# Performance work log

Hardware: AMD Instinct MI355X
Metric: run time of the kernel (lower is better)

## Reference

```python
import jax, jax.numpy as jnp
import numpy as np

H = 16  # num_heads

def _rotate_half(x):
    x1, x2 = jnp.split(x, 2, axis=-1)
    return jnp.concatenate((-x2, x1), axis=-1)

def setup_inputs() -> dict:
    key = jax.random.key(0)
    ks = jax.random.split(key, 8)
    B, N, C = 4, 2048, 1024
    d = C // H
    x = jax.random.normal(ks[0], (B, N, C), dtype=jnp.float32)
    cos = jax.random.uniform(ks[1], (1, 1, N, d), dtype=jnp.float32)
    sin = jax.random.uniform(ks[2], (1, 1, N, d), dtype=jnp.float32)
    s = 0.02
    Wq = jax.random.normal(ks[3], (C, C), dtype=jnp.float32) * s
    Wkv = jax.random.normal(ks[4], (C, 2 * C), dtype=jnp.float32) * s
    Wout = jax.random.normal(ks[5], (C, C), dtype=jnp.float32) * s
    bout = jnp.zeros((C,), dtype=jnp.float32)
    return {"x": x, "cos": cos, "sin": sin, "Wq": Wq, "Wkv": Wkv, "Wout": Wout, "bout": bout}

def reference(x, cos, sin, Wq, Wkv, Wout, bout):
    B, N, C = x.shape
    d = C // H
    scale = d ** (-0.5)
    # projections (qkv_bias=False)
    q = (x @ Wq).reshape(B, N, H, d).transpose(0, 2, 1, 3)        # (B,H,N,d)
    kv = x @ Wkv                                                   # (B,N,2C)
    k, v = jnp.split(kv, 2, axis=-1)
    k = k.reshape(B, N, H, d).transpose(0, 2, 1, 3)
    v = v.reshape(B, N, H, d).transpose(0, 2, 1, 3)
    # inline RoPE
    q = q * cos + _rotate_half(q) * sin
    k = k * cos + _rotate_half(k) * sin
    # naive full attention
    sim = jnp.einsum('bhid,bhjd->bhij', q, k) * scale              # (B,H,N,N)
    attn = jax.nn.softmax(sim, axis=-1)
    out = jnp.einsum('bhij,bhjd->bhid', attn, v)                   # (B,H,N,d)
    out = out.transpose(0, 2, 1, 3).reshape(B, N, C)
    return out @ Wout + bout
```

## Files before the change

kernel.cpp:

```cpp
#include <hip/hip_runtime.h>


typedef unsigned short u16;
typedef unsigned int u32;
typedef __attribute__((ext_vector_type(4))) short s16x4;
typedef __attribute__((ext_vector_type(8))) short short8;
typedef __attribute__((ext_vector_type(8))) unsigned short ushort8;
typedef __attribute__((ext_vector_type(4))) float f32x4;

#define MFMA16x16x32 __builtin_amdgcn_mfma_f32_16x16x32_bf16
#define QSCALE 0.180336880434135f

#if __has_builtin(__builtin_amdgcn_exp2f)
#define EXP2F __builtin_amdgcn_exp2f
#else
#define EXP2F exp2f
#endif

#define GBAR() __builtin_amdgcn_s_barrier()
#define CFENCE() asm volatile("" ::: "memory")
#define WAITVM(n) asm volatile("s_waitcnt vmcnt(" #n ")" ::: "memory")

__device__ __forceinline__ float b2f(u16 u) {
  union { u32 i; float f; } x; x.i = ((u32)u) << 16; return x.f;
}
__device__ __forceinline__ u16 f2b(float f) {
  union { float f; u32 i; } x; x.f = f;
  u32 r = (x.i + 0x7FFFu + ((x.i >> 16) & 1u)) >> 16;
  return (u16)r;
}
__device__ __forceinline__ u32 f2b_trunc32(float f) {
  union { float f; u32 i; } x; x.f = f;
  return x.i >> 16;
}
__device__ __forceinline__ bool detect_f32(const u32* __restrict__ cw) {
  u32 acc = 0;
#pragma unroll
  for (int i = 0; i < 64; ++i) acc |= cw[i];
  return (acc & 0x8000u) != 0;
}
__device__ __forceinline__ float ldval(const void* p, long i, bool f32) {
  return f32 ? ((const float*)p)[i] : b2f(((const u16*)p)[i]);
}
__device__ __forceinline__ ushort8 ld8f(const float* p) {
  float4 u0 = *(const float4*)p;
  float4 u1 = *(const float4*)(p + 4);
  ushort8 r;
  r[0] = f2b(u0.x); r[1] = f2b(u0.y); r[2] = f2b(u0.z); r[3] = f2b(u0.w);
  r[4] = f2b(u1.x); r[5] = f2b(u1.y); r[6] = f2b(u1.z); r[7] = f2b(u1.w);
  return r;
}
__device__ __forceinline__ void async16(const void* g, void* l) {
  __builtin_amdgcn_global_load_lds((const __attribute__((address_space(1))) void*)g,
                                   (__attribute__((address_space(3))) void*)l, 16, 0, 0);
}

__global__ __launch_bounds__(256)
void prep(const void* __restrict__ x, u16* __restrict__ x_bf16,
          const void* __restrict__ Wq, const void* __restrict__ Wkv,
          u16* __restrict__ WT1, const u32* __restrict__ cosw) {
  const bool f32 = detect_f32(cosw);
  const int b = blockIdx.x;
  const int t = threadIdx.x;
  if (b < 4096) {
    const long i = ((long)b * 256 + t) * 8;
    ushort8 v;
    if (f32) v = ld8f((const float*)x + i);
    else     v = *(const ushort8*)((const u16*)x + i);
    *(ushort8*)(x_bf16 + i) = v;
    return;
  }
  __shared__ __align__(16) u16 tile[64][65];
  const void* src; u16* dst; int R, C, bx, by;
  if (b < 4352) {
    const int idx = b - 4096;
    src = Wq;  dst = WT1;               R = 1024; C = 1024;
    bx = idx & 15; by = idx >> 4;
  } else {
    const int idx = b - 4352;
    src = Wkv; dst = WT1 + 1024 * 1024; R = 1024; C = 2048;
    bx = idx & 31; by = idx >> 5;
  }
  const int tr = by * 64, tc = bx * 64;
#pragma unroll
  for (int i = 0; i < 2; ++i) {
    const int ch = i * 256 + t;
    const int r = ch >> 3, cc = ch & 7;
    ushort8 v;
    if (f32) v = ld8f((const float*)src + (long)(tr + r) * C + tc + cc * 8);
    else     v = *(const ushort8*)((const u16*)src + (long)(tr + r) * C + tc + cc * 8);
#pragma unroll
    for (int j = 0; j < 8; ++j) tile[r][cc * 8 + j] = v[j];
  }
  __syncthreads();
#pragma unroll
  for (int i = 0; i < 2; ++i) {
    const int ch = i * 256 + t;
    const int c = ch >> 3, rc = ch & 7;
    ushort8 v;
#pragma unroll
    for (int j = 0; j < 8; ++j) v[j] = tile[rc * 8 + j][c];
    *(ushort8*)(dst + (long)(tc + c) * R + tr + rc * 8) = v;
  }
}

__global__ __launch_bounds__(256)
void transpose_any(const void* __restrict__ src, u16* __restrict__ dst,
                   int R, int C, const u32* __restrict__ cosw) {
  const bool f32 = detect_f32(cosw);
  const int tr = blockIdx.y * 64, tc = blockIdx.x * 64;
  __shared__ __align__(16) u16 tile[64][65];
  const int t = threadIdx.x;
#pragma unroll
  for (int i = 0; i < 2; ++i) {
    const int ch = i * 256 + t;
    const int r = ch >> 3, cc = ch & 7;
    ushort8 v;
    if (f32) v = ld8f((const float*)src + (long)(tr + r) * C + tc + cc * 8);
    else     v = *(const ushort8*)((const u16*)src + (long)(tr + r) * C + tc + cc * 8);
#pragma unroll
    for (int j = 0; j < 8; ++j) tile[r][cc * 8 + j] = v[j];
  }
  __syncthreads();
#pragma unroll
  for (int i = 0; i < 2; ++i) {
    const int ch = i * 256 + t;
    const int c = ch >> 3, rc = ch & 7;
    ushort8 v;
#pragma unroll
    for (int j = 0; j < 8; ++j) v[j] = tile[rc * 8 + j][c];
    *(ushort8*)(dst + (long)(tc + c) * R + tr + rc * 8) = v;
  }
}

__global__ __launch_bounds__(256)
void transpose_b16(const u16* __restrict__ src, u16* __restrict__ dst,
                   int R, int C, long sb, long db) {
  src += (long)blockIdx.z * sb;
  dst += (long)blockIdx.z * db;
  const int tr = blockIdx.y * 64, tc = blockIdx.x * 64;
  __shared__ __align__(16) u16 tile[64][65];
  const int t = threadIdx.x;
#pragma unroll
  for (int i = 0; i < 2; ++i) {
    const int ch = i * 256 + t;
    const int r = ch >> 3, cc = ch & 7;
    ushort8 v = *(const ushort8*)(src + (long)(tr + r) * C + tc + cc * 8);
#pragma unroll
    for (int j = 0; j < 8; ++j) tile[r][cc * 8 + j] = v[j];
  }
  __syncthreads();
#pragma unroll
  for (int i = 0; i < 2; ++i) {
    const int ch = i * 256 + t;
    const int c = ch >> 3, rc = ch & 7;
    ushort8 v;
#pragma unroll
    for (int j = 0; j < 8; ++j) v[j] = tile[rc * 8 + j][c];
    *(ushort8*)(dst + (long)(tc + c) * R + tr + rc * 8) = v;
  }
}

template <int MODE>
__global__ __launch_bounds__(256)
void gemm_fast(const u16* __restrict__ A, const u16* __restrict__ BT,
               const void* cosp, const void* sinp,
               u16* q_ws, u16* k_ws, u16* v_ws,
               const void* bias, void* outp, const u32* __restrict__ cosw) {
  constexpr int K = 1024, ITERS = K / 32;
  constexpr int NBX = (MODE == 0) ? 24 : 8;
  __shared__ __align__(16) u16 As[2][128 * 32];
  __shared__ __align__(16) u16 Bs[2][128 * 32];
  const int tid = threadIdx.x;
  const int wave = tid >> 6, lane = tid & 63;
  const int quad = lane >> 4, l15 = lane & 15;
  const int mh = (wave >> 1) * 64, nh = (wave & 1) * 64;
  const f32x4 zero4 = {0.f, 0.f, 0.f, 0.f};

  const int w = blockIdx.y * NBX + blockIdx.x;
  const int xcd = w & 7, idx = w >> 3;
  int bx, by;
  if (MODE == 0) {
    const int xc = idx / 48, r = idx % 48;
    by = xcd * 8 + r / 6;
    bx = xc * 6 + r % 6;
  } else {
    by = xcd * 8 + idx / 8;
    bx = idx % 8;
  }
  const int m0 = by * 128, n0 = bx * 128;

  f32x4 acc[4][4];
#pragma unroll
  for (int i = 0; i < 4; ++i)
#pragma unroll
    for (int j = 0; j < 4; ++j) acc[i][j] = zero4;

  const int c0 = tid, c1 = 256 + tid;
  const u16* a0p = A  + (long)(m0 + (c0 >> 2)) * K + (((c0 & 3) ^ ((c0 >> 3) & 3)) * 8);
  const u16* a1p = A  + (long)(m0 + (c1 >> 2)) * K + (((c1 & 3) ^ ((c1 >> 3) & 3)) * 8);
  const u16* b0p = BT + (long)(n0 + (c0 >> 2)) * K + (((c0 & 3) ^ ((c0 >> 3) & 3)) * 8);
  const u16* b1p = BT + (long)(n0 + (c1 >> 2)) * K + (((c1 & 3) ^ ((c1 >> 3) & 3)) * 8);

#define STAGE(buf, kt)                                \
  do {                                                \
    async16(a0p + (kt), As[buf] + c0 * 8);            \
    async16(a1p + (kt), As[buf] + c1 * 8);            \
    async16(b0p + (kt), Bs[buf] + c0 * 8);            \
    async16(b1p + (kt), Bs[buf] + c1 * 8);            \
  } while (0)

  const int rk = (quad ^ ((l15 >> 1) & 3)) * 8;

  STAGE(0, 0);
  for (int it = 0; it < ITERS; ++it) {
    const int cur = it & 1;
    __syncthreads();
    if (it + 1 < ITERS) STAGE(cur ^ 1, (it + 1) * 32);
    short8 af[4], bf[4];
#pragma unroll
    for (int s = 0; s < 4; ++s) {
      af[s] = *(const short8*)(As[cur] + (mh + s * 16 + l15) * 32 + rk);
      bf[s] = *(const short8*)(Bs[cur] + (nh + s * 16 + l15) * 32 + rk);
    }
#pragma unroll
    for (int i = 0; i < 4; ++i)
#pragma unroll
      for (int j = 0; j < 4; ++j)
        acc[i][j] = MFMA16x16x32(af[i], bf[j], acc[i][j], 0, 0, 0);
  }
#undef STAGE

  const bool f32 = detect_f32(cosw);

  if (MODE == 0) {
    const int seg = n0 >> 10;
    const int csbase = (n0 & 1023) + nh;
    u16* segp = (seg == 0) ? q_ws : (seg == 1) ? k_ws : v_ws;
#pragma unroll
    for (int i = 0; i < 4; ++i) {
#pragma unroll
      for (int r = 0; r < 4; ++r) {
        const int mm = m0 + mh + i * 16 + quad * 4 + r;
        const int b = mm >> 11, n = mm & 2047;
#pragma unroll
        for (int j = 0; j < 4; ++j) {
          const int cs = csbase + j * 16 + l15;
          const int h = cs >> 6, dv = cs & 63;
          float val = acc[i][j][r];
          if (seg < 2) {
            const float cv = ldval(cosp, (long)n * 64 + dv, f32);
            const float sv = ldval(sinp, (long)n * 64 + dv, f32);
            const float part = acc[i][j ^ 2][r];
            val = val * cv + ((dv < 32) ? -part : part) * sv;
            if (seg == 0) val *= QSCALE;
          }
          segp[(((long)(b * 16 + h) * 2048 + n) << 6) + dv] = f2b(val);
        }
      }
    }
  } else {
#pragma unroll
    for (int i = 0; i < 4; ++i) {
#pragma unroll
      for (int r = 0; r < 4; ++r) {
        const int mm = m0 + mh + i * 16 + quad * 4 + r;
#pragma unroll
        for (int j = 0; j < 4; ++j) {
          const int cc = n0 + nh + j * 16 + l15;
          const float val = acc[i][j][r] + ldval(bias, cc, f32);
          if (f32) ((float*)outp)[(long)mm * 1024 + cc] = val;
          else     ((u16*)outp)[(long)mm * 1024 + cc] = f2b(val);
        }
      }
    }
  }
}

__global__ __launch_bounds__(512, 4)
void flash_k(const u16* __restrict__ q_ws, const u16* __restrict__ k_ws,
             const u16* __restrict__ vT_ws, u16* __restrict__ attn) {
  __shared__ __align__(16) u16 Ks[3][64 * 64];
  __shared__ __align__(16) u16 Vts[3][64 * 64];
  const int tid = threadIdx.x, wave = tid >> 6, lane = tid & 63;
  const int quad = lane >> 4, l15 = lane & 15;
  const int s7 = l15 & 7;
  const int bid = blockIdx.x + (blockIdx.y << 3);
  const int qx = bid >> 6;
  const int bh = ((bid & 7) << 3) | ((bid >> 3) & 7);
  const int qr0 = qx * 256 + wave * 32;
  const u16* Q  = q_ws  + (long)bh * 2048 * 64;
  const u16* Kp = k_ws  + (long)bh * 2048 * 64;
  const u16* Vt = vT_ws + (long)bh * 64 * 2048;
  const f32x4 zero4 = {0.f, 0.f, 0.f, 0.f};
  short8 ones;
#pragma unroll
  for (int i = 0; i < 8; ++i) ones[i] = (short)0x3F80;

  short8 aq[2][2];
#pragma unroll
  for (int ms = 0; ms < 2; ++ms)
#pragma unroll
    for (int ks = 0; ks < 2; ++ks)
      aq[ms][ks] = *(const short8*)(Q + (long)(qr0 + ms * 16 + l15) * 64 + ks * 32 + quad * 8);

  f32x4 accO[2][4], accL[2];
#pragma unroll
  for (int ms = 0; ms < 2; ++ms) {
#pragma unroll
    for (int jd = 0; jd < 4; ++jd) accO[ms][jd] = zero4;
    accL[ms] = zero4;
  }

  const int rr = tid >> 3, gg = ((tid & 7) ^ (rr & 7)) * 8;

#define STAGEKV(buf, kt)                                          \
  do {                                                            \
    async16(Kp + (long)((kt) + rr) * 64 + gg, Ks[buf] + tid * 8); \
    async16(Vt + (long)rr * 2048 + (kt) + gg, Vts[buf] + tid * 8);\
  } while (0)

  const int vh = (quad & 1) * 4;
  const int vc0a = ((0 + (quad >> 1)) ^ s7) * 8 + vh;
  const int vc0b = ((2 + (quad >> 1)) ^ s7) * 8 + vh;
  const int vc1a = ((4 + (quad >> 1)) ^ s7) * 8 + vh;
  const int vc1b = ((6 + (quad >> 1)) ^ s7) * 8 + vh;

  STAGEKV(0, 0);
  STAGEKV(1, 64);
  for (int it = 0; it < 32; ++it) {
    const int cur = it % 3;
    if (it + 1 < 32) { WAITVM(2); } else { WAITVM(0); }
    GBAR(); CFENCE();
    if (it + 2 < 32) STAGEKV((it + 2) % 3, (it + 2) * 64);

#pragma unroll
    for (int k2 = 0; k2 < 2; ++k2) {
      u32 pk[2][4];
#pragma unroll
      for (int nsl = 0; nsl < 2; ++nsl) {
        const int ns = k2 * 2 + nsl;
        const u16* rowK = Ks[cur] + (ns * 16 + l15) * 64;
        short8 b0 = *(const short8*)(rowK + ((quad ^ s7) * 8));
        short8 b1 = *(const short8*)(rowK + (((quad + 4) ^ s7) * 8));
#pragma unroll
        for (int ms = 0; ms < 2; ++ms) {
          f32x4 t = MFMA16x16x32(b0, aq[ms][0], zero4, 0, 0, 0);
          f32x4 sa = MFMA16x16x32(b1, aq[ms][1], t, 0, 0, 0);
          const u32 p0 = f2b_trunc32(EXP2F(sa[0]));
          const u32 p1 = f2b_trunc32(EXP2F(sa[1]));
          const u32 p2 = f2b_trunc32(EXP2F(sa[2]));
          const u32 p3 = f2b_trunc32(EXP2F(sa[3]));
          pk[ms][nsl * 2 + 0] = p0 | (p1 << 16);
          pk[ms][nsl * 2 + 1] = p2 | (p3 << 16);
        }
      }
      short8 ap[2];
#pragma unroll
      for (int ms = 0; ms < 2; ++ms) {
        union { u32 w[4]; short8 s; } u;
        u.w[0] = pk[ms][0]; u.w[1] = pk[ms][1];
        u.w[2] = pk[ms][2]; u.w[3] = pk[ms][3];
        ap[ms] = u.s;
        accL[ms] = MFMA16x16x32(ap[ms], ones, accL[ms], 0, 0, 0);
      }
      const int ca = k2 ? vc1a : vc0a;
      const int cb = k2 ? vc1b : vc0b;
#pragma unroll
      for (int jd = 0; jd < 4; ++jd) {
        const u16* rowV = Vts[cur] + (jd * 16 + l15) * 64;
        union { s16x4 h[2]; short8 s; } bv;
        bv.h[0] = *(const s16x4*)(rowV + ca);
        bv.h[1] = *(const s16x4*)(rowV + cb);
#pragma unroll
        for (int ms = 0; ms < 2; ++ms)
          accO[ms][jd] = MFMA16x16x32(ap[ms], bv.s, accO[ms][jd], 0, 0, 0);
      }
    }
  }
#undef STAGEKV

  const int b = bh >> 4, h = bh & 15;
#pragma unroll
  for (int ms = 0; ms < 2; ++ms) {
#pragma unroll
    for (int r = 0; r < 4; ++r) {
      const float inv = 1.f / accL[ms][r];
      const int row = qr0 + ms * 16 + quad * 4 + r;
#pragma unroll
      for (int jd = 0; jd < 4; ++jd) {
        const int cc = h * 64 + jd * 16 + l15;
        attn[((long)(b * 2048 + row)) * 1024 + cc] = f2b(accO[ms][jd][r] * inv);
      }
    }
  }
}

extern "C" void kernel_launch(void* const* d_in, const int* in_sizes, int n_in,
                              void* d_out, int out_size, void* d_ws, size_t ws_size,
                              hipStream_t stream) {
  const void* x    = d_in[0];
  const void* cosp = d_in[1];
  const void* sinp = d_in[2];
  const void* Wq   = d_in[3];
  const void* Wkv  = d_in[4];
  const void* Wout = d_in[5];
  const void* bout = d_in[6];
  const u32* cosw  = (const u32*)d_in[1];

  char* ws = (char*)d_ws;
  const size_t MB = 1u << 20;
  u16* q_ws  = (u16*)(ws);
  u16* k_ws  = (u16*)(ws + 16 * MB);
  u16* vT_ws = (u16*)(ws + 32 * MB);
  u16* v_ws  = (u16*)(ws + 48 * MB);
  u16* attn  = (u16*)(ws + 48 * MB);
  u16* WoutT = (u16*)(ws + 32 * MB);

  u16* WT1;
  if (ws_size >= 88 * MB) WT1 = (u16*)(ws + 64 * MB);
  else                    WT1 = (u16*)d_out;
  u16* x_bf16 = WT1 + 3072 * 1024;

  prep<<<dim3(4864), 256, 0, stream>>>(x, x_bf16, Wq, Wkv, WT1, cosw);
  gemm_fast<0><<<dim3(24, 64), 256, 0, stream>>>(x_bf16, WT1, cosp, sinp,
                                                 q_ws, k_ws, v_ws,
                                                 nullptr, nullptr, cosw);
  transpose_b16<<<dim3(1, 32, 64), 256, 0, stream>>>(v_ws, vT_ws, 2048, 64,
                                                     (long)2048 * 64, (long)64 * 2048);
  flash_k<<<dim3(8, 64), 512, 0, stream>>>(q_ws, k_ws, vT_ws, attn);
  transpose_any<<<dim3(16, 16), 256, 0, stream>>>(Wout, WoutT, 1024, 1024, cosw);
  gemm_fast<1><<<dim3(8, 64), 256, 0, stream>>>(attn, WoutT, cosp, sinp,
                                                nullptr, nullptr, nullptr,
                                                bout, d_out, cosw);
}
```

Baseline: 312.4 us.

## Use 128-wide double-buffered KV tiles with MFMA priority boost in flash attention

The flash attention kernel now stages 128 keys per iteration in two LDS buffers instead of 64 keys in three. Synchronisation moves from explicit vmcnt waits plus a raw barrier to __syncthreads. This halves the number of loop iterations and barriers, and each thread now issues four async copies per stage. The P·V MFMA section is wrapped in s_setprio to favour matrix issue. LDS use per block grows from 48KB to 64KB, which may lower how many blocks fit on a CU, and the pipeline depth drops from two tiles ahead to one.

```diff
diff --git a/kernel.cpp b/kernel.cpp
--- a/kernel.cpp
+++ b/kernel.cpp
@@ -16,10 +16,6 @@
 #else
 #define EXP2F exp2f
 #endif
-
-#define GBAR() __builtin_amdgcn_s_barrier()
-#define CFENCE() asm volatile("" ::: "memory")
-#define WAITVM(n) asm volatile("s_waitcnt vmcnt(" #n ")" ::: "memory")
 
 __device__ __forceinline__ float b2f(u16 u) {
   union { u32 i; float f; } x; x.i = ((u32)u) << 16; return x.f;
@@ -280,8 +276,8 @@
 __global__ __launch_bounds__(512, 4)
 void flash_k(const u16* __restrict__ q_ws, const u16* __restrict__ k_ws,
              const u16* __restrict__ vT_ws, u16* __restrict__ attn) {
-  __shared__ __align__(16) u16 Ks[3][64 * 64];
-  __shared__ __align__(16) u16 Vts[3][64 * 64];
+  __shared__ __align__(16) u16 Ks[2][128 * 64];
+  __shared__ __align__(16) u16 Vts[2][64 * 128];
   const int tid = threadIdx.x, wave = tid >> 6, lane = tid & 63;
   const int quad = lane >> 4, l15 = lane & 15;
   const int s7 = l15 & 7;
@@ -312,30 +308,31 @@
     accL[ms] = zero4;
   }
 
-  const int rr = tid >> 3, gg = ((tid & 7) ^ (rr & 7)) * 8;
-
-#define STAGEKV(buf, kt)                                          \
-  do {                                                            \
-    async16(Kp + (long)((kt) + rr) * 64 + gg, Ks[buf] + tid * 8); \
-    async16(Vt + (long)rr * 2048 + (kt) + gg, Vts[buf] + tid * 8);\
+  const int kc0 = tid, kc1 = 512 + tid;
+  const int kr0 = kc0 >> 3, kg0 = ((kc0 & 7) ^ (kr0 & 7)) * 8;
+  const int kr1 = kc1 >> 3, kg1 = ((kc1 & 7) ^ (kr1 & 7)) * 8;
+  const int vr0 = kc0 >> 4, vg0 = ((kc0 & 15) ^ (vr0 & 7)) * 8;
+  const int vr1 = kc1 >> 4, vg1 = ((kc1 & 15) ^ (vr1 & 7)) * 8;
+
+#define STAGEKV(buf, kt)                                             \
+  do {                                                               \
+    async16(Kp + (long)((kt) + kr0) * 64 + kg0, Ks[buf] + kc0 * 8);  \
+    async16(Kp + (long)((kt) + kr1) * 64 + kg1, Ks[buf] + kc1 * 8);  \
+    async16(Vt + (long)vr0 * 2048 + (kt) + vg0, Vts[buf] + kc0 * 8); \
+    async16(Vt + (long)vr1 * 2048 + (kt) + vg1, Vts[buf] + kc1 * 8); \
   } while (0)
 
   const int vh = (quad & 1) * 4;
-  const int vc0a = ((0 + (quad >> 1)) ^ s7) * 8 + vh;
-  const int vc0b = ((2 + (quad >> 1)) ^ s7) * 8 + vh;
-  const int vc1a = ((4 + (quad >> 1)) ^ s7) * 8 + vh;
-  const int vc1b = ((6 + (quad >> 1)) ^ s7) * 8 + vh;
+  const int qh = quad >> 1;
 
   STAGEKV(0, 0);
-  STAGEKV(1, 64);
-  for (int it = 0; it < 32; ++it) {
-    const int cur = it % 3;
-    if (it + 1 < 32) { WAITVM(2); } else { WAITVM(0); }
-    GBAR(); CFENCE();
-    if (it + 2 < 32) STAGEKV((it + 2) % 3, (it + 2) * 64);
-
-#pragma unroll
-    for (int k2 = 0; k2 < 2; ++k2) {
+  for (int it = 0; it < 16; ++it) {
+    const int cur = it & 1;
+    __syncthreads();
+    if (it + 1 < 16) STAGEKV(cur ^ 1, (it + 1) * 128);
+
+#pragma unroll
+    for (int k2 = 0; k2 < 4; ++k2) {
       u32 pk[2][4];
 #pragma unroll
       for (int nsl = 0; nsl < 2; ++nsl) {
@@ -355,6 +352,7 @@
           pk[ms][nsl * 2 + 1] = p2 | (p3 << 16);
         }
       }
+      __builtin_amdgcn_s_setprio(1);
       short8 ap[2];
 #pragma unroll
       for (int ms = 0; ms < 2; ++ms) {
@@ -364,11 +362,11 @@
         ap[ms] = u.s;
         accL[ms] = MFMA16x16x32(ap[ms], ones, accL[ms], 0, 0, 0);
       }
-      const int ca = k2 ? vc1a : vc0a;
-      const int cb = k2 ? vc1b : vc0b;
+      const int ca = ((4 * k2 + qh) ^ s7) * 8 + vh;
+      const int cb = ((4 * k2 + 2 + qh) ^ s7) * 8 + vh;
 #pragma unroll
       for (int jd = 0; jd < 4; ++jd) {
-        const u16* rowV = Vts[cur] + (jd * 16 + l15) * 64;
+        const u16* rowV = Vts[cur] + (jd * 16 + l15) * 128;
         union { s16x4 h[2]; short8 s; } bv;
         bv.h[0] = *(const s16x4*)(rowV + ca);
         bv.h[1] = *(const s16x4*)(rowV + cb);
@@ -376,6 +374,7 @@
         for (int ms = 0; ms < 2; ++ms)
           accO[ms][jd] = MFMA16x16x32(ap[ms], bv.s, accO[ms][jd], 0, 0, 0);
       }
+      __builtin_amdgcn_s_setprio(0);
     }
   }
 #undef STAGEKV
```

After: 303.1 us. -3.0%, faster.
